# Kernel tuning notes

Measured on AMD Instinct MI355X. Metric: run time of the kernel, lower is better.

## Reference

```python
import jax, jax.numpy as jnp
import numpy as np

B, T, D = 2, 2048, 512
H, W = 8, 32
d = D // H


def setup_inputs() -> dict:
    key = jax.random.key(0)
    ks = jax.random.split(key, 9)
    s = 1.0 / np.sqrt(D)
    return {
        "x": jax.random.normal(ks[0], (B, T, D), dtype=jnp.float32),
        "wq": jax.random.normal(ks[1], (D, D), dtype=jnp.float32) * s,
        "bq": jnp.zeros((D,), dtype=jnp.float32),
        "wk": jax.random.normal(ks[2], (D, D), dtype=jnp.float32) * s,
        "bk": jnp.zeros((D,), dtype=jnp.float32),
        "wv": jax.random.normal(ks[3], (D, D), dtype=jnp.float32) * s,
        "bv": jnp.zeros((D,), dtype=jnp.float32),
        "wo": jax.random.normal(ks[4], (D, D), dtype=jnp.float32) * s,
        "bo": jnp.zeros((D,), dtype=jnp.float32),
    }


def _local_attn(x, wq, bq, wk, bk, wv, bv, wo, bo):
    Bx, Tx, Dx = x.shape
    # projections (weights stored as [D_in, D_out])
    Q = (x @ wq + bq).reshape(Bx, Tx, H, d).transpose(0, 2, 1, 3)  # [B,H,T,d]
    K = (x @ wk + bk).reshape(Bx, Tx, H, d).transpose(0, 2, 1, 3)
    V = (x @ wv + bv).reshape(Bx, Tx, H, d).transpose(0, 2, 1, 3)
    # zero-pad time axis by W on both sides (matches F.pad value=0; NO masking,
    # padded zero keys get score 0 and participate in softmax like the original)
    Kp = jnp.pad(K, ((0, 0), (0, 0), (W, W), (0, 0)))  # [B,H,T+2W,d]
    Vp = jnp.pad(V, ((0, 0), (0, 0), (W, W), (0, 0)))
    idx = jnp.arange(Tx)[:, None] + jnp.arange(2 * W + 1)[None, :]  # [T, 2W+1]
    K_loc = Kp[:, :, idx, :]  # [B,H,T,2W+1,d]
    V_loc = Vp[:, :, idx, :]
    scores = jnp.einsum("bhtd,bhtwd->bhtw", Q, K_loc) / jnp.sqrt(jnp.asarray(d, x.dtype))
    attn = jax.nn.softmax(scores, axis=-1)
    out = jnp.einsum("bhtw,bhtwd->bhtd", attn, V_loc)  # [B,H,T,d]
    out = out.transpose(0, 2, 1, 3).reshape(Bx, Tx, Dx)
    return out @ wo + bo


def reference(x, wq, bq, wk, bk, wv, bv, wo, bo):
    return _local_attn(x, wq, bq, wk, bk, wv, bv, wo, bo)
```

## Files before the change

kernel.cpp:

```cpp
#include <hip/hip_runtime.h>

using f16x8 = __attribute__((ext_vector_type(8))) _Float16;
using f16x4 = __attribute__((ext_vector_type(4))) _Float16;
using f32x4 = __attribute__((ext_vector_type(4))) float;

#define T_SEQ 2048
#define D_MODEL 512
#define NH 8
#define HD 64
#define NB 2
#define M_ROWS (NB * T_SEQ)

#define GLOAD_LDS16(g, l)                                              \
  __builtin_amdgcn_global_load_lds(                                    \
      (const __attribute__((address_space(1))) void*)(g),              \
      (__attribute__((address_space(3))) void*)(l), 16, 0, 0)

__global__ __launch_bounds__(256) void cvt_all(
    const float* __restrict__ x, const float* __restrict__ wq,
    const float* __restrict__ wk, const float* __restrict__ wv,
    const float* __restrict__ wo, const float* __restrict__ bq,
    const float* __restrict__ bk, const float* __restrict__ bv,
    _Float16* __restrict__ xh, _Float16* __restrict__ wT,
    float* __restrict__ bias3) {
  int bid = blockIdx.x;
  int i = threadIdx.x;
  if (bid < 2048) {
    int idx = (bid * 256 + i) * 4;
    float4 v = *(const float4*)(x + idx);
    f16x4 h;
    h[0] = (_Float16)v.x; h[1] = (_Float16)v.y;
    h[2] = (_Float16)v.z; h[3] = (_Float16)v.w;
    *(f16x4*)(xh + idx) = h;
    return;
  }
  bid -= 2048;
  const int z = bid >> 8;
  const int by = (bid >> 4) & 15;
  const int bx = bid & 15;
  const float* w = z == 0 ? wq : z == 1 ? wk : z == 2 ? wv : wo;
  __shared__ float t[32][33];
  int r0 = by * 32, c0 = bx * 32;
#pragma unroll
  for (int p = 0; p < 4; ++p) {
    int e = p * 256 + i;
    int row = e >> 5, col = e & 31;
    t[row][col] = w[(size_t)(r0 + row) * D_MODEL + c0 + col];
  }
  __syncthreads();
  _Float16* o = wT + (size_t)z * D_MODEL * D_MODEL;
#pragma unroll
  for (int p = 0; p < 4; ++p) {
    int e = p * 256 + i;
    int orow = e >> 5, ocol = e & 31;
    o[(size_t)(c0 + orow) * D_MODEL + r0 + ocol] = (_Float16)t[ocol][orow];
  }
  if (bx == 0 && by == 0 && z < 3) {
    const float* bb = z == 0 ? bq : z == 1 ? bk : bv;
#pragma unroll
    for (int p = 0; p < 2; ++p)
      bias3[z * D_MODEL + p * 256 + i] = bb[p * 256 + i];
  }
}

template <int OUT_F32>
__global__ __launch_bounds__(256) void gemm_bt(
    const _Float16* __restrict__ A, const _Float16* __restrict__ BtBase,
    const float* __restrict__ biasBase, void* outBase) {
  const int z = blockIdx.z;
  const _Float16* Bt = BtBase + (size_t)z * D_MODEL * D_MODEL;
  const float* bias = biasBase + z * D_MODEL;
  const int m0 = blockIdx.y * 128;
  const int n0 = blockIdx.x * 128;
  __shared__ _Float16 At[128 * 32];
  __shared__ _Float16 Bts[128 * 32];
  const int tid = threadIdx.x;
  const int l = tid & 63;
  const int wv = tid >> 6;
  const int wm = wv >> 1, wn = wv & 1;
  const int r16 = l & 15, g4 = l >> 4;
  f32x4 acc[4][4] = {};
  for (int k0 = 0; k0 < D_MODEL; k0 += 32) {
#pragma unroll
    for (int cc = 0; cc < 2; ++cc) {
      int c = tid + cc * 256;
      int row = c >> 2, part = c & 3;
      int wbase = (wv * 64 + cc * 256) * 8;
      GLOAD_LDS16(&A[(size_t)(m0 + row) * D_MODEL + k0 + part * 8],
                  &At[wbase]);
      GLOAD_LDS16(&Bt[(size_t)(n0 + row) * D_MODEL + k0 + part * 8],
                  &Bts[wbase]);
    }
    __syncthreads();
    f16x8 a[4], b[4];
#pragma unroll
    for (int mf = 0; mf < 4; ++mf)
      a[mf] = *(const f16x8*)&At[(wm * 64 + mf * 16 + r16) * 32 + g4 * 8];
#pragma unroll
    for (int nf = 0; nf < 4; ++nf)
      b[nf] = *(const f16x8*)&Bts[(wn * 64 + nf * 16 + r16) * 32 + g4 * 8];
#pragma unroll
    for (int mf = 0; mf < 4; ++mf)
#pragma unroll
      for (int nf = 0; nf < 4; ++nf)
        acc[mf][nf] = __builtin_amdgcn_mfma_f32_16x16x32_f16(
            a[mf], b[nf], acc[mf][nf], 0, 0, 0);
    __syncthreads();
  }
#pragma unroll
  for (int mf = 0; mf < 4; ++mf) {
#pragma unroll
    for (int nf = 0; nf < 4; ++nf) {
      int col = n0 + wn * 64 + nf * 16 + r16;
      float bs = bias[col];
#pragma unroll
      for (int r = 0; r < 4; ++r) {
        int rowi = m0 + wm * 64 + mf * 16 + g4 * 4 + r;
        float v = acc[mf][nf][r] + bs;
        if (OUT_F32)
          ((float*)outBase)[(size_t)rowi * D_MODEL + col] = v;
        else
          ((_Float16*)outBase)[(size_t)z * M_ROWS * D_MODEL +
                               (size_t)rowi * D_MODEL + col] = (_Float16)v;
      }
    }
  }
}

__global__ __launch_bounds__(256) void local_attn(
    const _Float16* __restrict__ Q, const _Float16* __restrict__ K,
    const _Float16* __restrict__ V, _Float16* __restrict__ att) {
  const int t0 = blockIdx.x * 64;
  const int h = blockIdx.y;
  const int b = blockIdx.z;
  const int k0 = t0 - 32;
  __shared__ _Float16 Qs[64 * 64];
  __shared__ _Float16 Ks[128 * 64];
  __shared__ _Float16 Vt[64 * 128];
  __shared__ _Float16 Ps[64 * 128];
  const int tid = threadIdx.x;
  const int l = tid & 63;
  const int wv = tid >> 6;
  const size_t colbase = (size_t)h * HD;
#pragma unroll
  for (int cc = 0; cc < 2; ++cc) {
    int c = tid + cc * 256;
    int row = c >> 3, part = c & 7;
    GLOAD_LDS16(&Q[(size_t)(b * T_SEQ + t0 + row) * D_MODEL + colbase + part * 8],
                &Qs[(wv * 64 + cc * 256) * 8]);
  }
  const bool interior = (k0 >= 0) && (k0 + 128 <= T_SEQ);
  if (interior) {
#pragma unroll
    for (int cc = 0; cc < 4; ++cc) {
      int c = tid + cc * 256;
      int row = c >> 3, part = c & 7;
      GLOAD_LDS16(&K[(size_t)(b * T_SEQ + k0 + row) * D_MODEL + colbase + part * 8],
                  &Ks[(wv * 64 + cc * 256) * 8]);
    }
  } else {
#pragma unroll
    for (int cc = 0; cc < 4; ++cc) {
      int c = tid + cc * 256;
      int row = c >> 3, part = c & 7;
      int t = k0 + row;
      f16x8 v = {};
      if (t >= 0 && t < T_SEQ)
        v = *(const f16x8*)&K[(size_t)(b * T_SEQ + t) * D_MODEL + colbase + part * 8];
      *(f16x8*)&Ks[row * 64 + part * 8] = v;
    }
  }
#pragma unroll
  for (int cc = 0; cc < 4; ++cc) {
    int c = tid + cc * 256;
    int row = c >> 3, part = c & 7;
    int t = k0 + row;
    f16x8 v = {};
    if (t >= 0 && t < T_SEQ)
      v = *(const f16x8*)&V[(size_t)(b * T_SEQ + t) * D_MODEL + colbase + part * 8];
#pragma unroll
    for (int j = 0; j < 8; ++j) Vt[(part * 8 + j) * 128 + row] = v[j];
  }
  __syncthreads();
  const int r16 = l & 15, g4 = l >> 4;
  f32x4 s[8] = {};
#pragma unroll
  for (int kk = 0; kk < 2; ++kk) {
    f16x8 a = *(const f16x8*)&Qs[(wv * 16 + r16) * 64 + kk * 32 + g4 * 8];
#pragma unroll
    for (int nf = 0; nf < 8; ++nf) {
      f16x8 bb = *(const f16x8*)&Ks[(nf * 16 + r16) * 64 + kk * 32 + g4 * 8];
      s[nf] = __builtin_amdgcn_mfma_f32_16x16x32_f16(a, bb, s[nf], 0, 0, 0);
    }
  }
#pragma unroll
  for (int r = 0; r < 4; ++r) {
    int ql = wv * 16 + g4 * 4 + r;
    float vals[8];
    float m = -1e30f;
#pragma unroll
    for (int nf = 0; nf < 8; ++nf) {
      int j = nf * 16 + r16;
      bool in = (j >= ql) && (j <= ql + 64);
      float sv = in ? s[nf][r] * 0.125f : -1e30f;
      vals[nf] = sv;
      m = fmaxf(m, sv);
    }
#pragma unroll
    for (int off = 1; off < 16; off <<= 1) m = fmaxf(m, __shfl_xor(m, off, 64));
    float e[8];
    float sum = 0.f;
#pragma unroll
    for (int nf = 0; nf < 8; ++nf) {
      float ev = (vals[nf] > -1e29f) ? __expf(vals[nf] - m) : 0.f;
      e[nf] = ev;
      sum += ev;
    }
#pragma unroll
    for (int off = 1; off < 16; off <<= 1) sum += __shfl_xor(sum, off, 64);
    float inv = 1.f / sum;
#pragma unroll
    for (int nf = 0; nf < 8; ++nf)
      Ps[ql * 128 + nf * 16 + r16] = (_Float16)(e[nf] * inv);
  }
  __syncthreads();
  f32x4 o[4] = {};
#pragma unroll
  for (int kk = 0; kk < 4; ++kk) {
    f16x8 a = *(const f16x8*)&Ps[(wv * 16 + r16) * 128 + kk * 32 + g4 * 8];
#pragma unroll
    for (int nf = 0; nf < 4; ++nf) {
      f16x8 bb = *(const f16x8*)&Vt[(nf * 16 + r16) * 128 + kk * 32 + g4 * 8];
      o[nf] = __builtin_amdgcn_mfma_f32_16x16x32_f16(a, bb, o[nf], 0, 0, 0);
    }
  }
#pragma unroll
  for (int nf = 0; nf < 4; ++nf)
#pragma unroll
    for (int r = 0; r < 4; ++r) {
      int row = t0 + wv * 16 + g4 * 4 + r;
      int col = nf * 16 + r16;
      att[(size_t)(b * T_SEQ + row) * D_MODEL + colbase + col] =
          (_Float16)o[nf][r];
    }
}

extern "C" void kernel_launch(void* const* d_in, const int* in_sizes, int n_in,
                              void* d_out, int out_size, void* d_ws,
                              size_t ws_size, hipStream_t stream) {
  const float* x = (const float*)d_in[0];
  const float* wq = (const float*)d_in[1];
  const float* bq = (const float*)d_in[2];
  const float* wk = (const float*)d_in[3];
  const float* bk = (const float*)d_in[4];
  const float* wv = (const float*)d_in[5];
  const float* bv = (const float*)d_in[6];
  const float* wo = (const float*)d_in[7];
  const float* bo = (const float*)d_in[8];

  char* ws = (char*)d_ws;
  _Float16* xh = (_Float16*)(ws);
  _Float16* wT = (_Float16*)(ws + (4 << 20));
  float* bias3 = (float*)(ws + (6 << 20));
  _Float16* QKV = (_Float16*)(ws + (6 << 20) + (64 << 10));
  _Float16* att = xh;

  cvt_all<<<3072, 256, 0, stream>>>(x, wq, wk, wv, wo, bq, bk, bv, xh, wT,
                                    bias3);
  gemm_bt<0><<<dim3(4, 32, 3), 256, 0, stream>>>(xh, wT, bias3, QKV);
  const _Float16* Qm = QKV;
  const _Float16* Km = QKV + (size_t)M_ROWS * D_MODEL;
  const _Float16* Vm = Km + (size_t)M_ROWS * D_MODEL;
  local_attn<<<dim3(32, 8, 2), 256, 0, stream>>>(Qm, Km, Vm, att);
  gemm_bt<1><<<dim3(4, 32, 1), 256, 0, stream>>>(
      att, wT + (size_t)3 * D_MODEL * D_MODEL, bo, d_out);
}
```

Baseline: 51.01 us.

## Fuse local attention with output projection and double-buffer QKV GEMM

Merges the local attention kernel and the output-projection GEMM into one kernel. Each block handles 16 query rows across all heads, with each wave processing two heads, and keeps the attention output in LDS before multiplying by the transposed output weights. This removes one launch and the global round trip of the attention tensor. In exchange, each block reads the whole output weight matrix straight from global memory and shrinks the key window from 128 to 80 keys per 16 queries. The QKV GEMM also gains a double-buffered LDS pipeline so the next k-tile is loaded while the current one is computed.

```diff
diff --git a/kernel.cpp b/kernel.cpp
--- a/kernel.cpp
+++ b/kernel.cpp
@@ -63,48 +63,57 @@
   }
 }
 
-template <int OUT_F32>
-__global__ __launch_bounds__(256) void gemm_bt(
+__global__ __launch_bounds__(256) void gemm_qkv(
     const _Float16* __restrict__ A, const _Float16* __restrict__ BtBase,
-    const float* __restrict__ biasBase, void* outBase) {
+    const float* __restrict__ biasBase, _Float16* __restrict__ outBase) {
+  constexpr int NT = D_MODEL / 32;
   const int z = blockIdx.z;
   const _Float16* Bt = BtBase + (size_t)z * D_MODEL * D_MODEL;
   const float* bias = biasBase + z * D_MODEL;
   const int m0 = blockIdx.y * 128;
   const int n0 = blockIdx.x * 128;
-  __shared__ _Float16 At[128 * 32];
-  __shared__ _Float16 Bts[128 * 32];
+  __shared__ _Float16 At[2][128 * 32];
+  __shared__ _Float16 Bts[2][128 * 32];
   const int tid = threadIdx.x;
   const int l = tid & 63;
   const int wv = tid >> 6;
   const int wm = wv >> 1, wn = wv & 1;
   const int r16 = l & 15, g4 = l >> 4;
   f32x4 acc[4][4] = {};
-  for (int k0 = 0; k0 < D_MODEL; k0 += 32) {
+
+  auto stage = [&](int bb, int k0) {
 #pragma unroll
     for (int cc = 0; cc < 2; ++cc) {
       int c = tid + cc * 256;
       int row = c >> 2, part = c & 3;
-      int wbase = (wv * 64 + cc * 256) * 8;
       GLOAD_LDS16(&A[(size_t)(m0 + row) * D_MODEL + k0 + part * 8],
-                  &At[wbase]);
+                  &At[bb][(c - l) * 8]);
       GLOAD_LDS16(&Bt[(size_t)(n0 + row) * D_MODEL + k0 + part * 8],
-                  &Bts[wbase]);
-    }
-    __syncthreads();
+                  &Bts[bb][(c - l) * 8]);
+    }
+  };
+  auto compute = [&](int bb) {
     f16x8 a[4], b[4];
 #pragma unroll
     for (int mf = 0; mf < 4; ++mf)
-      a[mf] = *(const f16x8*)&At[(wm * 64 + mf * 16 + r16) * 32 + g4 * 8];
+      a[mf] = *(const f16x8*)&At[bb][(wm * 64 + mf * 16 + r16) * 32 + g4 * 8];
 #pragma unroll
     for (int nf = 0; nf < 4; ++nf)
-      b[nf] = *(const f16x8*)&Bts[(wn * 64 + nf * 16 + r16) * 32 + g4 * 8];
+      b[nf] = *(const f16x8*)&Bts[bb][(wn * 64 + nf * 16 + r16) * 32 + g4 * 8];
 #pragma unroll
     for (int mf = 0; mf < 4; ++mf)
 #pragma unroll
       for (int nf = 0; nf < 4; ++nf)
         acc[mf][nf] = __builtin_amdgcn_mfma_f32_16x16x32_f16(
             a[mf], b[nf], acc[mf][nf], 0, 0, 0);
+  };
+
+  stage(0, 0);
+  __syncthreads();
+#pragma unroll
+  for (int t = 0; t < NT; ++t) {
+    if (t + 1 < NT) stage((t + 1) & 1, (t + 1) * 32);
+    compute(t & 1);
     __syncthreads();
   }
 #pragma unroll
@@ -116,133 +125,141 @@
 #pragma unroll
       for (int r = 0; r < 4; ++r) {
         int rowi = m0 + wm * 64 + mf * 16 + g4 * 4 + r;
-        float v = acc[mf][nf][r] + bs;
-        if (OUT_F32)
-          ((float*)outBase)[(size_t)rowi * D_MODEL + col] = v;
-        else
-          ((_Float16*)outBase)[(size_t)z * M_ROWS * D_MODEL +
-                               (size_t)rowi * D_MODEL + col] = (_Float16)v;
-      }
-    }
-  }
-}
-
-__global__ __launch_bounds__(256) void local_attn(
+        outBase[(size_t)z * M_ROWS * D_MODEL + (size_t)rowi * D_MODEL + col] =
+            (_Float16)(acc[mf][nf][r] + bs);
+      }
+    }
+  }
+}
+
+__global__ __launch_bounds__(256) void attn_out(
     const _Float16* __restrict__ Q, const _Float16* __restrict__ K,
-    const _Float16* __restrict__ V, _Float16* __restrict__ att) {
-  const int t0 = blockIdx.x * 64;
-  const int h = blockIdx.y;
-  const int b = blockIdx.z;
+    const _Float16* __restrict__ V, const _Float16* __restrict__ woT,
+    const float* __restrict__ bo, float* __restrict__ out) {
+  constexpr int VT_H = 64 * 96;
+  constexpr int PS_H = 16 * 96;
+  constexpr int ATT_STRIDE = 520;
+  __shared__ __align__(16) _Float16 smem[4 * VT_H + 4 * PS_H + 16 * ATT_STRIDE];
+  const int t0 = blockIdx.x * 16;
+  const int b = blockIdx.y;
   const int k0 = t0 - 32;
-  __shared__ _Float16 Qs[64 * 64];
-  __shared__ _Float16 Ks[128 * 64];
-  __shared__ _Float16 Vt[64 * 128];
-  __shared__ _Float16 Ps[64 * 128];
   const int tid = threadIdx.x;
   const int l = tid & 63;
   const int wv = tid >> 6;
-  const size_t colbase = (size_t)h * HD;
-#pragma unroll
-  for (int cc = 0; cc < 2; ++cc) {
-    int c = tid + cc * 256;
-    int row = c >> 3, part = c & 7;
-    GLOAD_LDS16(&Q[(size_t)(b * T_SEQ + t0 + row) * D_MODEL + colbase + part * 8],
-                &Qs[(wv * 64 + cc * 256) * 8]);
-  }
-  const bool interior = (k0 >= 0) && (k0 + 128 <= T_SEQ);
-  if (interior) {
-#pragma unroll
-    for (int cc = 0; cc < 4; ++cc) {
-      int c = tid + cc * 256;
-      int row = c >> 3, part = c & 7;
-      GLOAD_LDS16(&K[(size_t)(b * T_SEQ + k0 + row) * D_MODEL + colbase + part * 8],
-                  &Ks[(wv * 64 + cc * 256) * 8]);
-    }
-  } else {
-#pragma unroll
-    for (int cc = 0; cc < 4; ++cc) {
-      int c = tid + cc * 256;
-      int row = c >> 3, part = c & 7;
-      int t = k0 + row;
+  const int r16 = l & 15, g4 = l >> 4;
+  _Float16* Vt = smem + wv * VT_H;
+  _Float16* Ps = smem + 4 * VT_H + wv * PS_H;
+  _Float16* attL = smem + 4 * VT_H + 4 * PS_H;
+
+  {
+    f16x8 zz = {};
+    *(f16x8*)&Vt[l * 96 + 80] = zz;
+    *(f16x8*)&Vt[l * 96 + 88] = zz;
+    if (l < 32) *(f16x8*)&Ps[(l >> 1) * 96 + 80 + (l & 1) * 8] = zz;
+  }
+
+  for (int hi = 0; hi < 2; ++hi) {
+    const int h = wv * 2 + hi;
+    const size_t cb = (size_t)h * HD;
+#pragma unroll
+    for (int j = 0; j < 10; ++j) {
+      int c = l + j * 64;
+      int key = c >> 3, part = c & 7;
+      int t = k0 + key;
       f16x8 v = {};
       if (t >= 0 && t < T_SEQ)
-        v = *(const f16x8*)&K[(size_t)(b * T_SEQ + t) * D_MODEL + colbase + part * 8];
-      *(f16x8*)&Ks[row * 64 + part * 8] = v;
-    }
-  }
-#pragma unroll
-  for (int cc = 0; cc < 4; ++cc) {
-    int c = tid + cc * 256;
-    int row = c >> 3, part = c & 7;
-    int t = k0 + row;
-    f16x8 v = {};
-    if (t >= 0 && t < T_SEQ)
-      v = *(const f16x8*)&V[(size_t)(b * T_SEQ + t) * D_MODEL + colbase + part * 8];
-#pragma unroll
-    for (int j = 0; j < 8; ++j) Vt[(part * 8 + j) * 128 + row] = v[j];
+        v = *(const f16x8*)&V[(size_t)(b * T_SEQ + t) * D_MODEL + cb +
+                              part * 8];
+#pragma unroll
+      for (int jj = 0; jj < 8; ++jj) Vt[(part * 8 + jj) * 96 + key] = v[jj];
+    }
+    f32x4 s[5] = {};
+#pragma unroll
+    for (int ks = 0; ks < 2; ++ks) {
+      f16x8 a = *(const f16x8*)&Q[(size_t)(b * T_SEQ + t0 + r16) * D_MODEL +
+                                  cb + ks * 32 + g4 * 8];
+#pragma unroll
+      for (int nf = 0; nf < 5; ++nf) {
+        int t = k0 + nf * 16 + r16;
+        f16x8 bb = {};
+        if (t >= 0 && t < T_SEQ)
+          bb = *(const f16x8*)&K[(size_t)(b * T_SEQ + t) * D_MODEL + cb +
+                                 ks * 32 + g4 * 8];
+        s[nf] = __builtin_amdgcn_mfma_f32_16x16x32_f16(a, bb, s[nf], 0, 0, 0);
+      }
+    }
+#pragma unroll
+    for (int r = 0; r < 4; ++r) {
+      int q = g4 * 4 + r;
+      float vals[5];
+      float m = -1e30f;
+#pragma unroll
+      for (int nf = 0; nf < 5; ++nf) {
+        int j = nf * 16 + r16;
+        bool in = (j >= q) && (j <= q + 64);
+        float sv = in ? s[nf][r] * 0.125f : -1e30f;
+        vals[nf] = sv;
+        m = fmaxf(m, sv);
+      }
+#pragma unroll
+      for (int off = 1; off < 16; off <<= 1)
+        m = fmaxf(m, __shfl_xor(m, off, 64));
+      float e[5];
+      float sum = 0.f;
+#pragma unroll
+      for (int nf = 0; nf < 5; ++nf) {
+        float ev = (vals[nf] > -1e29f) ? __expf(vals[nf] - m) : 0.f;
+        e[nf] = ev;
+        sum += ev;
+      }
+#pragma unroll
+      for (int off = 1; off < 16; off <<= 1) sum += __shfl_xor(sum, off, 64);
+      float inv = 1.f / sum;
+#pragma unroll
+      for (int nf = 0; nf < 5; ++nf)
+        Ps[q * 96 + nf * 16 + r16] = (_Float16)(e[nf] * inv);
+    }
+    f32x4 o[4] = {};
+#pragma unroll
+    for (int ks = 0; ks < 3; ++ks) {
+      f16x8 a = *(const f16x8*)&Ps[r16 * 96 + ks * 32 + g4 * 8];
+#pragma unroll
+      for (int nf = 0; nf < 4; ++nf) {
+        f16x8 bb = *(const f16x8*)&Vt[(nf * 16 + r16) * 96 + ks * 32 + g4 * 8];
+        o[nf] = __builtin_amdgcn_mfma_f32_16x16x32_f16(a, bb, o[nf], 0, 0, 0);
+      }
+    }
+#pragma unroll
+    for (int nf = 0; nf < 4; ++nf)
+#pragma unroll
+      for (int r = 0; r < 4; ++r)
+        attL[(g4 * 4 + r) * ATT_STRIDE + h * HD + nf * 16 + r16] =
+            (_Float16)o[nf][r];
   }
   __syncthreads();
-  const int r16 = l & 15, g4 = l >> 4;
-  f32x4 s[8] = {};
-#pragma unroll
-  for (int kk = 0; kk < 2; ++kk) {
-    f16x8 a = *(const f16x8*)&Qs[(wv * 16 + r16) * 64 + kk * 32 + g4 * 8];
-#pragma unroll
-    for (int nf = 0; nf < 8; ++nf) {
-      f16x8 bb = *(const f16x8*)&Ks[(nf * 16 + r16) * 64 + kk * 32 + g4 * 8];
-      s[nf] = __builtin_amdgcn_mfma_f32_16x16x32_f16(a, bb, s[nf], 0, 0, 0);
-    }
-  }
-#pragma unroll
-  for (int r = 0; r < 4; ++r) {
-    int ql = wv * 16 + g4 * 4 + r;
-    float vals[8];
-    float m = -1e30f;
-#pragma unroll
-    for (int nf = 0; nf < 8; ++nf) {
-      int j = nf * 16 + r16;
-      bool in = (j >= ql) && (j <= ql + 64);
-      float sv = in ? s[nf][r] * 0.125f : -1e30f;
-      vals[nf] = sv;
-      m = fmaxf(m, sv);
-    }
-#pragma unroll
-    for (int off = 1; off < 16; off <<= 1) m = fmaxf(m, __shfl_xor(m, off, 64));
-    float e[8];
-    float sum = 0.f;
-#pragma unroll
-    for (int nf = 0; nf < 8; ++nf) {
-      float ev = (vals[nf] > -1e29f) ? __expf(vals[nf] - m) : 0.f;
-      e[nf] = ev;
-      sum += ev;
-    }
-#pragma unroll
-    for (int off = 1; off < 16; off <<= 1) sum += __shfl_xor(sum, off, 64);
-    float inv = 1.f / sum;
+  f32x4 acc[8] = {};
+  const int nbase = wv * 128;
+  for (int kk = 0; kk < 16; ++kk) {
+    f16x8 a = *(const f16x8*)&attL[r16 * ATT_STRIDE + kk * 32 + g4 * 8];
+    f16x8 bfr[8];
 #pragma unroll
     for (int nf = 0; nf < 8; ++nf)
-      Ps[ql * 128 + nf * 16 + r16] = (_Float16)(e[nf] * inv);
-  }
-  __syncthreads();
-  f32x4 o[4] = {};
-#pragma unroll
-  for (int kk = 0; kk < 4; ++kk) {
-    f16x8 a = *(const f16x8*)&Ps[(wv * 16 + r16) * 128 + kk * 32 + g4 * 8];
-#pragma unroll
-    for (int nf = 0; nf < 4; ++nf) {
-      f16x8 bb = *(const f16x8*)&Vt[(nf * 16 + r16) * 128 + kk * 32 + g4 * 8];
-      o[nf] = __builtin_amdgcn_mfma_f32_16x16x32_f16(a, bb, o[nf], 0, 0, 0);
-    }
-  }
-#pragma unroll
-  for (int nf = 0; nf < 4; ++nf)
-#pragma unroll
-    for (int r = 0; r < 4; ++r) {
-      int row = t0 + wv * 16 + g4 * 4 + r;
-      int col = nf * 16 + r16;
-      att[(size_t)(b * T_SEQ + row) * D_MODEL + colbase + col] =
-          (_Float16)o[nf][r];
-    }
+      bfr[nf] = *(const f16x8*)&woT[(size_t)(nbase + nf * 16 + r16) * D_MODEL +
+                                    kk * 32 + g4 * 8];
+#pragma unroll
+    for (int nf = 0; nf < 8; ++nf)
+      acc[nf] = __builtin_amdgcn_mfma_f32_16x16x32_f16(a, bfr[nf], acc[nf],
+                                                       0, 0, 0);
+  }
+#pragma unroll
+  for (int nf = 0; nf < 8; ++nf) {
+    int col = nbase + nf * 16 + r16;
+    float bs = bo[col];
+#pragma unroll
+    for (int r = 0; r < 4; ++r)
+      out[(size_t)(b * T_SEQ + t0 + g4 * 4 + r) * D_MODEL + col] =
+          acc[nf][r] + bs;
+  }
 }
 
 extern "C" void kernel_launch(void* const* d_in, const int* in_sizes, int n_in,
@@ -263,15 +280,13 @@
   _Float16* wT = (_Float16*)(ws + (4 << 20));
   float* bias3 = (float*)(ws + (6 << 20));
   _Float16* QKV = (_Float16*)(ws + (6 << 20) + (64 << 10));
-  _Float16* att = xh;
 
   cvt_all<<<3072, 256, 0, stream>>>(x, wq, wk, wv, wo, bq, bk, bv, xh, wT,
                                     bias3);
-  gemm_bt<0><<<dim3(4, 32, 3), 256, 0, stream>>>(xh, wT, bias3, QKV);
+  gemm_qkv<<<dim3(4, 32, 3), 256, 0, stream>>>(xh, wT, bias3, QKV);
   const _Float16* Qm = QKV;
   const _Float16* Km = QKV + (size_t)M_ROWS * D_MODEL;
   const _Float16* Vm = Km + (size_t)M_ROWS * D_MODEL;
-  local_attn<<<dim3(32, 8, 2), 256, 0, stream>>>(Qm, Km, Vm, att);
-  gemm_bt<1><<<dim3(4, 32, 1), 256, 0, stream>>>(
-      att, wT + (size_t)3 * D_MODEL * D_MODEL, bo, d_out);
-}
+  attn_out<<<dim3(T_SEQ / 16, NB), 256, 0, stream>>>(
+      Qm, Km, Vm, wT + (size_t)3 * D_MODEL * D_MODEL, bo, (float*)d_out);
+}
```

Measured after the change: 54.98 us. +7.8%, slower.
